# Kernel tuning notes

Hardware: AMD Instinct MI355X
Metric: run time of the kernel (lower is better)

The kernel has to match this reference:

```python
import jax, jax.numpy as jnp
import numpy as np

B, C, H, W = 16, 256, 64, 64
NH, HD, NM = 4, 32, 4  # heads, head_dim, memory tokens
HID = NH * HD


def rms_norm(x, g):
    # F.normalize(x, dim=1) * sqrt(C) * g  (channel dim = 1)
    norm = jnp.maximum(jnp.linalg.norm(x, axis=1, keepdims=True), 1e-12)
    return x / norm * (x.shape[1] ** 0.5) * g


def setup_inputs() -> dict:
    key = jax.random.key(0)
    ks = jax.random.split(key, 5)
    return {
        "x": jax.random.normal(ks[0], (B, C, H, W), jnp.float32),
        "g_in": jnp.ones((1, C, 1, 1), jnp.float32),
        "mem_kv": jax.random.normal(ks[1], (2, NH, HD, NM), jnp.float32),
        "w_qkv": jax.random.normal(ks[2], (HID * 3, C), jnp.float32) * (C ** -0.5),
        "w_out": jax.random.normal(ks[3], (C, HID), jnp.float32) * (HID ** -0.5),
        "b_out": jnp.zeros((C,), jnp.float32),
        "g_out": jnp.ones((1, C, 1, 1), jnp.float32),
    }


def reference(x, g_in, mem_kv, w_qkv, w_out, b_out, g_out):
    b, c, h, w = x.shape
    n = h * w
    scale = HD ** -0.5

    xn = rms_norm(x, g_in)
    # 1x1 conv as matmul over channel dim: [B, 3*HID, H, W]
    qkv = jnp.einsum('oc,bchw->bohw', w_qkv, xn)
    q, k, v = jnp.split(qkv, 3, axis=1)
    # b (h d) x y -> b h d n
    q = q.reshape(b, NH, HD, n)
    k = k.reshape(b, NH, HD, n)
    v = v.reshape(b, NH, HD, n)

    # prepend memory key/value tokens: [b, h, d, NM + n]
    mk = jnp.broadcast_to(mem_kv[0], (b, NH, HD, NM))
    mv = jnp.broadcast_to(mem_kv[1], (b, NH, HD, NM))
    k = jnp.concatenate([mk, k], axis=-1)
    v = jnp.concatenate([mv, v], axis=-1)

    q = jax.nn.softmax(q, axis=-2) * scale  # softmax over head_dim
    k = jax.nn.softmax(k, axis=-1)          # softmax over tokens

    context = jnp.einsum('bhdn,bhen->bhde', k, v)  # [b, h, d, e]
    out = jnp.einsum('bhde,bhdn->bhen', context, q)  # [b, h, e, n]
    out = out.reshape(b, HID, h, w)

    out = jnp.einsum('oc,bchw->bohw', w_out, out) + b_out[None, :, None, None]
    return rms_norm(out, g_out)
```

## Files before the change

kernel.cpp:

```cpp
#include <hip/hip_runtime.h>
#include <math.h>

typedef unsigned short u16;
typedef unsigned int u32;

#define NBATCH 16
#define NCH    256
#define NPIX   4096
#define NHEAD  4
#define HDIM   32
#define NMEM   4
#define HID    128
#define OC3    384
#define SCALE_Q 0.17677669529663687f

typedef __bf16 bf16x8 __attribute__((ext_vector_type(8)));
typedef float  f32x4  __attribute__((ext_vector_type(4)));

__device__ __forceinline__ u16 bfb(float f){
  union { __bf16 h; u16 u; } x; x.h = (__bf16)f; return x.u;
}
__device__ __forceinline__ u32 pkbf2(float a, float b){
  union { __bf16 h[2]; u32 u; } x; x.h[0] = (__bf16)a; x.h[1] = (__bf16)b; return x.u;
}
__device__ __forceinline__ void gload_lds16(const void* gp, void* lp){
  __builtin_amdgcn_global_load_lds(
      (const __attribute__((address_space(1))) unsigned int*)gp,
      (__attribute__((address_space(3))) unsigned int*)lp, 16, 0, 0);
}

__global__ __launch_bounds__(256) void k_pack(const float* __restrict__ wqkv,
                                              const float* __restrict__ gin,
                                              const float* __restrict__ wout,
                                              const float* __restrict__ memkv,
                                              u16* __restrict__ wqb,
                                              u16* __restrict__ wob,
                                              float* __restrict__ ctxmem,
                                              float* __restrict__ zmem)
{
  int i = blockIdx.x*256 + threadIdx.x;
  if (i < OC3*NCH){ int c = i & 255; wqb[i] = bfb(wqkv[i]*gin[c]); }
  else if (i < OC3*NCH + NCH*HID){ int j = i - OC3*NCH; wob[j] = bfb(wout[j]); }
  else {
    int j = i - (OC3*NCH + NCH*HID);
    if (j < 4096){
      int h = j>>10, d = (j>>5)&31, e = j&31;
      float s = 0.f;
      #pragma unroll
      for (int m=0;m<4;m++)
        s += __expf(memkv[(h*HDIM+d)*NMEM + m]) * memkv[512 + (h*HDIM+e)*NMEM + m];
      ctxmem[j] = s;
    } else if (j < 4224){
      int k = j - 4096; int h = k>>5, d = k&31;
      float s = 0.f;
      #pragma unroll
      for (int m=0;m<4;m++) s += __expf(memkv[(h*HDIM+d)*NMEM + m]);
      zmem[k] = s;
    }
  }
}

__global__ __launch_bounds__(512, 4) void k_qkvx(const float* __restrict__ x,
                                                 const u16* __restrict__ wqb,
                                                 u16* __restrict__ qt,
                                                 float* __restrict__ ctxp2)
{
  __shared__ __align__(16) char smem[52480];
  float (*Xs)[64]   = (float(*)[64])smem;
  u16*   Bx         = (u16*)(smem + 16384);
  float (*ssqp)[64] = (float(*)[64])(smem + 50176);
  float* rl         = (float*)(smem + 52224);
  u16*   Ek         = (u16*)smem;
  u16*   Vv         = (u16*)(smem + 18432);
  float (*psx)[64]  = (float(*)[64])(smem + 36864);

  const int t = threadIdx.x, w = t>>6, lane = t&63;
  const int n0 = blockIdx.x*64, b = blockIdx.y;
  const int qw = lane>>4, rr = lane&15;

  {
    float ssq = 0.f;
    for (int s=0;s<4;++s){
      asm volatile("s_waitcnt lgkmcnt(0)" ::: "memory");
      const float* gp = x + ((size_t)b*NCH + s*64 + w*8 + (lane>>4))*NPIX + n0 + (lane&15)*4;
      gload_lds16(gp,                    &Xs[w*8 + 0][0]);
      gload_lds16(gp + (size_t)4*NPIX,   &Xs[w*8 + 4][0]);
      asm volatile("s_waitcnt vmcnt(0)" ::: "memory");
      u32 pk[4];
      #pragma unroll
      for (int q=0;q<4;q++){
        float v0 = Xs[w*8 + 2*q    ][lane];
        float v1 = Xs[w*8 + 2*q + 1][lane];
        ssq += v0*v0 + v1*v1;
        pk[q] = pkbf2(v0, v1);
      }
      *(int4*)&Bx[lane*264 + s*64 + w*8] = make_int4((int)pk[0],(int)pk[1],(int)pk[2],(int)pk[3]);
    }
    ssqp[w][lane] = ssq;
  }
  __syncthreads();
  if (t < 64){
    float s = 0.f;
    #pragma unroll
    for (int g=0;g<8;g++) s += ssqp[g][t];
    rl[t] = 16.0f / fmaxf(sqrtf(s), 1e-12f);
  }

  f32x4 acc[3][4];
  #pragma unroll
  for (int p=0;p<3;p++)
    #pragma unroll
    for (int nf=0;nf<4;nf++) acc[p][nf] = (f32x4){0.f,0.f,0.f,0.f};

  const u16* aw = wqb + (size_t)(w*16 + rr)*NCH + qw*8;
  bf16x8 caf0 = *(const bf16x8*)(aw);
  bf16x8 caf1 = *(const bf16x8*)(aw + 128*NCH);
  bf16x8 caf2 = *(const bf16x8*)(aw + 256*NCH);
  #pragma unroll
  for (int c0=0; c0<NCH; c0+=32){
    bf16x8 bfr[4];
    #pragma unroll
    for (int nf=0;nf<4;nf++)
      bfr[nf] = *(const bf16x8*)&Bx[(nf*16+rr)*264 + c0 + qw*8];
    bf16x8 naf0 = caf0, naf1 = caf1, naf2 = caf2;
    if (c0 < NCH-32){
      naf0 = *(const bf16x8*)(aw + c0+32);
      naf1 = *(const bf16x8*)(aw + 128*NCH + c0+32);
      naf2 = *(const bf16x8*)(aw + 256*NCH + c0+32);
    }
    #pragma unroll
    for (int nf=0;nf<4;nf++){
      acc[0][nf] = __builtin_amdgcn_mfma_f32_16x16x32_bf16(caf0, bfr[nf], acc[0][nf], 0, 0, 0);
      acc[1][nf] = __builtin_amdgcn_mfma_f32_16x16x32_bf16(bfr[nf], caf1, acc[1][nf], 0, 0, 0);
      acc[2][nf] = __builtin_amdgcn_mfma_f32_16x16x32_bf16(bfr[nf], caf2, acc[2][nf], 0, 0, 0);
    }
    caf0 = naf0; caf1 = naf1; caf2 = naf2;
  }

  __syncthreads();

  float zk = 0.f;
  #pragma unroll
  for (int nf=0;nf<4;nf++){
    const float4 rv4 = *(const float4*)&rl[nf*16 + qw*4];
    float e0 = __expf(acc[1][nf][0]*rv4.x);
    float e1 = __expf(acc[1][nf][1]*rv4.y);
    float e2 = __expf(acc[1][nf][2]*rv4.z);
    float e3 = __expf(acc[1][nf][3]*rv4.w);
    zk += e0+e1+e2+e3;
    *(int2*)&Ek[(w*16+rr)*72 + nf*16 + qw*4] =
        make_int2((int)pkbf2(e0,e1), (int)pkbf2(e2,e3));
    float v0 = acc[2][nf][0]*rv4.x, v1 = acc[2][nf][1]*rv4.y;
    float v2 = acc[2][nf][2]*rv4.z, v3 = acc[2][nf][3]*rv4.w;
    *(int2*)&Vv[(w*16+rr)*72 + nf*16 + qw*4] =
        make_int2((int)pkbf2(v0,v1), (int)pkbf2(v2,v3));
  }
  zk += __shfl_xor(zk, 16, 64);
  zk += __shfl_xor(zk, 32, 64);

  float qv[4][4], pm[4], ps[4];
  #pragma unroll
  for (int nf=0;nf<4;nf++){
    float rv = rl[nf*16 + rr];
    float m = -1e30f;
    #pragma unroll
    for (int r=0;r<4;r++){ qv[nf][r] = acc[0][nf][r]*rv; m = fmaxf(m, qv[nf][r]); }
    m = fmaxf(m, __shfl_xor(m, 16, 64));
    m = fmaxf(m, __shfl_xor(m, 32, 64));
    float s = 0.f;
    #pragma unroll
    for (int r=0;r<4;r++){ qv[nf][r] = __expf(qv[nf][r]-m); s += qv[nf][r]; }
    s += __shfl_xor(s, 16, 64);
    s += __shfl_xor(s, 32, 64);
    pm[nf] = m; ps[nf] = s;
  }
  if (lane < 16){
    #pragma unroll
    for (int nf=0;nf<4;nf++){ ssqp[w][nf*16+lane] = pm[nf]; psx[w][nf*16+lane] = ps[nf]; }
  }
  __syncthreads();
  {
    const int pw = w^1;
    u16* qbase = qt + ((size_t)b*NPIX + n0)*HID + w*16 + qw*4;
    #pragma unroll
    for (int nf=0;nf<4;nf++){
      float om = ssqp[pw][nf*16+rr], os = psx[pw][nf*16+rr];
      float M = fmaxf(pm[nf], om);
      float S = ps[nf]*__expf(pm[nf]-M) + os*__expf(om-M);
      float f = __expf(pm[nf]-M) * SCALE_Q / S;
      u32 lo = pkbf2(qv[nf][0]*f, qv[nf][1]*f);
      u32 hi = pkbf2(qv[nf][2]*f, qv[nf][3]*f);
      *(int2*)(qbase + (size_t)(nf*16+rr)*HID) = make_int2((int)lo,(int)hi);
    }
  }

  {
    const int h = w>>1, eh = w&1;
    f32x4 pacc[2] = {(f32x4){0.f,0.f,0.f,0.f},(f32x4){0.f,0.f,0.f,0.f}};
    #pragma unroll
    for (int ks=0; ks<2; ks++){
      bf16x8 bv = *(const bf16x8*)&Vv[(h*32+eh*16+rr)*72 + ks*32 + qw*8];
      #pragma unroll
      for (int i=0;i<2;i++){
        bf16x8 ae = *(const bf16x8*)&Ek[(h*32+i*16+rr)*72 + ks*32 + qw*8];
        pacc[i] = __builtin_amdgcn_mfma_f32_16x16x32_bf16(ae, bv, pacc[i], 0, 0, 0);
      }
    }
    float* pb = ctxp2 + ((size_t)((b*64 + blockIdx.x)*4 + h))*1088;
    #pragma unroll
    for (int i=0;i<2;i++)
      #pragma unroll
      for (int reg=0;reg<4;reg++)
        pb[(i*16+qw*4+reg)*32 + eh*16 + rr] = pacc[i][reg];
    if (qw==0) pb[1024 + (w&1)*16 + rr] = zk;
  }
}

__global__ __launch_bounds__(256) void k_w2(const float* __restrict__ ctxp2,
                                            const float* __restrict__ ctxmem,
                                            const float* __restrict__ zmem,
                                            const u16* __restrict__ wob,
                                            u16* __restrict__ w2b)
{
  __shared__ u16 Ct[32][40];
  __shared__ float zps[8][32];
  __shared__ float rinv[32];
  const int bh = blockIdx.x, b = bh>>2, h = bh&3;
  const int t = threadIdx.x, w = t>>6, lane = t&63;
  const int qw = lane>>4, rr = lane&15;
  const int d = t>>3, e0 = (t&7)*4;

  const float* base = ctxp2 + ((size_t)(b*64)*4 + h)*1088;
  float4 ps = make_float4(0.f,0.f,0.f,0.f);
  for (int s=0;s<64;s++){
    float4 v = *(const float4*)(base + (size_t)s*4*1088 + d*32 + e0);
    ps.x+=v.x; ps.y+=v.y; ps.z+=v.z; ps.w+=v.w;
  }
  {
    int dz = t&31, sg = t>>5;
    float zp = 0.f;
    for (int s=sg*8; s<sg*8+8; s++) zp += base[(size_t)s*4*1088 + 1024 + dz];
    zps[sg][dz] = zp;
  }
  __syncthreads();
  if (t < 32){
    float z = zmem[h*32 + t];
    #pragma unroll
    for (int g=0;g<8;g++) z += zps[g][t];
    rinv[t] = 1.0f / z;
  }
  __syncthreads();
  {
    float ri = rinv[d];
    const float* cm = ctxmem + h*1024 + d*32 + e0;
    Ct[d][e0+0] = bfb((ps.x + cm[0])*ri);
    Ct[d][e0+1] = bfb((ps.y + cm[1])*ri);
    Ct[d][e0+2] = bfb((ps.z + cm[2])*ri);
    Ct[d][e0+3] = bfb((ps.w + cm[3])*ri);
  }
  __syncthreads();
  f32x4 pacc[4][2];
  #pragma unroll
  for (int mf=0;mf<4;mf++)
    #pragma unroll
    for (int nd=0;nd<2;nd++) pacc[mf][nd] = (f32x4){0.f,0.f,0.f,0.f};
  bf16x8 be[2];
  be[0] = *(const bf16x8*)&Ct[rr][qw*8];
  be[1] = *(const bf16x8*)&Ct[16+rr][qw*8];
  #pragma unroll
  for (int mf=0;mf<4;mf++){
    bf16x8 af = *(const bf16x8*)&wob[(size_t)(w*64+mf*16+rr)*HID + h*32 + qw*8];
    #pragma unroll
    for (int nd=0;nd<2;nd++)
      pacc[mf][nd] = __builtin_amdgcn_mfma_f32_16x16x32_bf16(af, be[nd], pacc[mf][nd], 0, 0, 0);
  }
  #pragma unroll
  for (int mf=0;mf<4;mf++)
    #pragma unroll
    for (int nd=0;nd<2;nd++)
      #pragma unroll
      for (int reg=0;reg<4;reg++)
        w2b[((size_t)b*NCH + w*64+mf*16+qw*4+reg)*HID + h*32 + nd*16 + rr] =
            bfb(pacc[mf][nd][reg]);
}

__global__ __launch_bounds__(256) void k_fout(const u16* __restrict__ qt,
                                              const u16* __restrict__ w2b,
                                              const float* __restrict__ bout,
                                              const float* __restrict__ gout,
                                              float* __restrict__ out)
{
  __shared__ float ssql[4][64];
  const int t = threadIdx.x, w = t>>6, lane = t&63;
  const int n0 = blockIdx.x*64, b = blockIdx.y;
  const int qw = lane>>4, rr = lane&15;

  f32x4 acc[4][4];
  #pragma unroll
  for (int i=0;i<4;i++)
    #pragma unroll
    for (int j=0;j<4;j++) acc[i][j] = (f32x4){0.f,0.f,0.f,0.f};

  const u16* qbase = qt + ((size_t)b*NPIX + n0)*HID;
  const u16* wbase = w2b + (size_t)b*NCH*HID;
  #pragma unroll
  for (int k0=0;k0<HID;k0+=32){
    bf16x8 bq[4], aw[4];
    #pragma unroll
    for (int nf=0;nf<4;nf++)
      bq[nf] = *(const bf16x8*)(qbase + (size_t)(nf*16+rr)*HID + k0 + qw*8);
    #pragma unroll
    for (int mf=0;mf<4;mf++)
      aw[mf] = *(const bf16x8*)(wbase + (size_t)(w*64+mf*16+rr)*HID + k0 + qw*8);
    #pragma unroll
    for (int mf=0;mf<4;mf++)
      #pragma unroll
      for (int nf=0;nf<4;nf++)
        acc[mf][nf] = __builtin_amdgcn_mfma_f32_16x16x32_bf16(bq[nf], aw[mf], acc[mf][nf], 0, 0, 0);
  }
  float psq[4][4] = {{0.f}};
  #pragma unroll
  for (int mf=0;mf<4;mf++){
    float bb = bout[w*64+mf*16+rr];
    #pragma unroll
    for (int nf=0;nf<4;nf++)
      #pragma unroll
      for (int reg=0;reg<4;reg++){
        float v = acc[mf][nf][reg] + bb;
        acc[mf][nf][reg] = v;
        psq[nf][reg] += v*v;
      }
  }
  #pragma unroll
  for (int nf=0;nf<4;nf++)
    #pragma unroll
    for (int reg=0;reg<4;reg++){
      psq[nf][reg] += __shfl_xor(psq[nf][reg], 1, 64);
      psq[nf][reg] += __shfl_xor(psq[nf][reg], 2, 64);
      psq[nf][reg] += __shfl_xor(psq[nf][reg], 4, 64);
      psq[nf][reg] += __shfl_xor(psq[nf][reg], 8, 64);
    }
  if (rr==0){
    #pragma unroll
    for (int nf=0;nf<4;nf++)
      #pragma unroll
      for (int reg=0;reg<4;reg++)
        ssql[w][nf*16+qw*4+reg] = psq[nf][reg];
  }
  __syncthreads();
  float4 rv4[4];
  #pragma unroll
  for (int nf=0;nf<4;nf++){
    float4 s0 = *(const float4*)&ssql[0][nf*16+qw*4];
    float4 s1 = *(const float4*)&ssql[1][nf*16+qw*4];
    float4 s2 = *(const float4*)&ssql[2][nf*16+qw*4];
    float4 s3 = *(const float4*)&ssql[3][nf*16+qw*4];
    rv4[nf].x = 16.0f / fmaxf(sqrtf(s0.x+s1.x+s2.x+s3.x), 1e-12f);
    rv4[nf].y = 16.0f / fmaxf(sqrtf(s0.y+s1.y+s2.y+s3.y), 1e-12f);
    rv4[nf].z = 16.0f / fmaxf(sqrtf(s0.z+s1.z+s2.z+s3.z), 1e-12f);
    rv4[nf].w = 16.0f / fmaxf(sqrtf(s0.w+s1.w+s2.w+s3.w), 1e-12f);
  }
  #pragma unroll
  for (int mf=0;mf<4;mf++){
    float g = gout[w*64+mf*16+rr];
    float* po = out + ((size_t)(b*NCH + w*64+mf*16+rr))*NPIX + n0;
    #pragma unroll
    for (int nf=0;nf<4;nf++){
      float4 o4;
      o4.x = acc[mf][nf][0]*rv4[nf].x*g;
      o4.y = acc[mf][nf][1]*rv4[nf].y*g;
      o4.z = acc[mf][nf][2]*rv4[nf].z*g;
      o4.w = acc[mf][nf][3]*rv4[nf].w*g;
      *(float4*)(po + nf*16 + qw*4) = o4;
    }
  }
}

extern "C" void kernel_launch(void* const* d_in, const int* in_sizes, int n_in,
                              void* d_out, int out_size, void* d_ws, size_t ws_size,
                              hipStream_t stream)
{
  const float* x     = (const float*)d_in[0];
  const float* gin   = (const float*)d_in[1];
  const float* memkv = (const float*)d_in[2];
  const float* wqkv  = (const float*)d_in[3];
  const float* wout  = (const float*)d_in[4];
  const float* bout  = (const float*)d_in[5];
  const float* gout  = (const float*)d_in[6];
  float* out = (float*)d_out;

  char* ws = (char*)d_ws;
  u16*    qt     = (u16*)   (ws);
  float*  ctxp2  = (float*) (ws + 16777216);
  u16*    w2b    = (u16*)   (ws + 34603008);
  float*  ctxmem = (float*) (ws + 35651584);
  float*  zmem   = (float*) (ws + 35667968);
  u16*    wqb    = (u16*)   (ws + 35668480);
  u16*    wob    = (u16*)   (ws + 35865088);

  hipLaunchKernelGGL(k_pack, dim3(529),   dim3(256), 0, stream,
                     wqkv, gin, wout, memkv, wqb, wob, ctxmem, zmem);
  hipLaunchKernelGGL(k_qkvx, dim3(64,16), dim3(512), 0, stream, x, wqb, qt, ctxp2);
  hipLaunchKernelGGL(k_w2,   dim3(64),    dim3(256), 0, stream,
                     ctxp2, ctxmem, zmem, wob, w2b);
  hipLaunchKernelGGL(k_fout, dim3(64,16), dim3(256), 0, stream,
                     qt, w2b, bout, gout, out);
}
```

Baseline: 178.8 us.

## Fuse context reduction into qkv kernel via last-block atomic, apply context in output kernel

Removes the separate k_w2 launch. The last block per batch, found with an atomic counter reset in k_pack, now reduces the partial contexts into a normalized bf16 context in k_qkvx. k_fout now applies context to q per head with MFMA, stages the result in LDS, then multiplies by w_out, instead of using a precomputed per-batch fused weight. This saves one kernel launch and the serialized small-grid k_w2. In exchange k_fout does extra MFMA and LDS work, and the tail block in k_qkvx carries a serial reduction.

```diff
diff --git a/kernel.cpp b/kernel.cpp
--- a/kernel.cpp
+++ b/kernel.cpp
@@ -36,7 +36,8 @@
                                               u16* __restrict__ wqb,
                                               u16* __restrict__ wob,
                                               float* __restrict__ ctxmem,
-                                              float* __restrict__ zmem)
+                                              float* __restrict__ zmem,
+                                              u32* __restrict__ cnt)
 {
   int i = blockIdx.x*256 + threadIdx.x;
   if (i < OC3*NCH){ int c = i & 255; wqb[i] = bfb(wqkv[i]*gin[c]); }
@@ -56,6 +57,8 @@
       #pragma unroll
       for (int m=0;m<4;m++) s += __expf(memkv[(h*HDIM+d)*NMEM + m]);
       zmem[k] = s;
+    } else if (j < 4240){
+      cnt[j-4224] = 0;
     }
   }
 }
@@ -63,7 +66,11 @@
 __global__ __launch_bounds__(512, 4) void k_qkvx(const float* __restrict__ x,
                                                  const u16* __restrict__ wqb,
                                                  u16* __restrict__ qt,
-                                                 float* __restrict__ ctxp2)
+                                                 float* __restrict__ ctxp2,
+                                                 const float* __restrict__ ctxmem,
+                                                 const float* __restrict__ zmem,
+                                                 u16* __restrict__ ctxn,
+                                                 u32* __restrict__ cnt)
 {
   __shared__ __align__(16) char smem[52480];
   float (*Xs)[64]   = (float(*)[64])smem;
@@ -73,6 +80,7 @@
   u16*   Ek         = (u16*)smem;
   u16*   Vv         = (u16*)(smem + 18432);
   float (*psx)[64]  = (float(*)[64])(smem + 36864);
+  __shared__ int lflag;
 
   const int t = threadIdx.x, w = t>>6, lane = t&63;
   const int n0 = blockIdx.x*64, b = blockIdx.y;
@@ -214,109 +222,109 @@
         pb[(i*16+qw*4+reg)*32 + eh*16 + rr] = pacc[i][reg];
     if (qw==0) pb[1024 + (w&1)*16 + rr] = zk;
   }
-}
-
-__global__ __launch_bounds__(256) void k_w2(const float* __restrict__ ctxp2,
-                                            const float* __restrict__ ctxmem,
-                                            const float* __restrict__ zmem,
-                                            const u16* __restrict__ wob,
-                                            u16* __restrict__ w2b)
-{
-  __shared__ u16 Ct[32][40];
-  __shared__ float zps[8][32];
-  __shared__ float rinv[32];
-  const int bh = blockIdx.x, b = bh>>2, h = bh&3;
-  const int t = threadIdx.x, w = t>>6, lane = t&63;
-  const int qw = lane>>4, rr = lane&15;
-  const int d = t>>3, e0 = (t&7)*4;
-
-  const float* base = ctxp2 + ((size_t)(b*64)*4 + h)*1088;
-  float4 ps = make_float4(0.f,0.f,0.f,0.f);
-  for (int s=0;s<64;s++){
-    float4 v = *(const float4*)(base + (size_t)s*4*1088 + d*32 + e0);
-    ps.x+=v.x; ps.y+=v.y; ps.z+=v.z; ps.w+=v.w;
-  }
+
+  __threadfence();
+  __syncthreads();
+  if (t == 0){
+    u32 old = __hip_atomic_fetch_add(cnt + b, 1u, __ATOMIC_ACQ_REL,
+                                     __HIP_MEMORY_SCOPE_AGENT);
+    lflag = (old == 63);
+  }
+  __syncthreads();
+  if (!lflag) return;
+  __threadfence();
+
+  float* rl2 = (float*)ssqp;
+  float (*zps)[128] = (float(*)[128])psx;
+  const float* cb = ctxp2 + (size_t)(b*64)*4*1088;
   {
-    int dz = t&31, sg = t>>5;
-    float zp = 0.f;
-    for (int s=sg*8; s<sg*8+8; s++) zp += base[(size_t)s*4*1088 + 1024 + dz];
-    zps[sg][dz] = zp;
-  }
-  __syncthreads();
-  if (t < 32){
-    float z = zmem[h*32 + t];
-    #pragma unroll
-    for (int g=0;g<8;g++) z += zps[g][t];
-    rinv[t] = 1.0f / z;
-  }
-  __syncthreads();
-  {
-    float ri = rinv[d];
-    const float* cm = ctxmem + h*1024 + d*32 + e0;
-    Ct[d][e0+0] = bfb((ps.x + cm[0])*ri);
-    Ct[d][e0+1] = bfb((ps.y + cm[1])*ri);
-    Ct[d][e0+2] = bfb((ps.z + cm[2])*ri);
-    Ct[d][e0+3] = bfb((ps.w + cm[3])*ri);
-  }
-  __syncthreads();
-  f32x4 pacc[4][2];
-  #pragma unroll
-  for (int mf=0;mf<4;mf++)
-    #pragma unroll
-    for (int nd=0;nd<2;nd++) pacc[mf][nd] = (f32x4){0.f,0.f,0.f,0.f};
-  bf16x8 be[2];
-  be[0] = *(const bf16x8*)&Ct[rr][qw*8];
-  be[1] = *(const bf16x8*)&Ct[16+rr][qw*8];
-  #pragma unroll
-  for (int mf=0;mf<4;mf++){
-    bf16x8 af = *(const bf16x8*)&wob[(size_t)(w*64+mf*16+rr)*HID + h*32 + qw*8];
-    #pragma unroll
-    for (int nd=0;nd<2;nd++)
-      pacc[mf][nd] = __builtin_amdgcn_mfma_f32_16x16x32_bf16(af, be[nd], pacc[mf][nd], 0, 0, 0);
-  }
-  #pragma unroll
-  for (int mf=0;mf<4;mf++)
-    #pragma unroll
-    for (int nd=0;nd<2;nd++)
-      #pragma unroll
-      for (int reg=0;reg<4;reg++)
-        w2b[((size_t)b*NCH + w*64+mf*16+qw*4+reg)*HID + h*32 + nd*16 + rr] =
-            bfb(pacc[mf][nd][reg]);
+    int sg = t>>7, idx = t&127;
+    int h = idx>>5, dd = idx&31;
+    const float* pz = cb + (size_t)h*1088 + 1024 + dd;
+    float zs = 0.f;
+    #pragma unroll
+    for (int s=0;s<16;s++) zs += pz[(size_t)(sg*16+s)*4*1088];
+    zps[sg][idx] = zs;
+  }
+  __syncthreads();
+  if (t < 128) rl2[t] = 1.0f/(zps[0][t]+zps[1][t]+zps[2][t]+zps[3][t]+zmem[t]);
+  __syncthreads();
+  #pragma unroll
+  for (int uu=0; uu<2; ++uu){
+    int u = t + uu*512;
+    int h = u>>8, dd = (u>>3)&31, e0 = (u&7)*4;
+    const float* pp = cb + (size_t)h*1088 + dd*32 + e0;
+    const float* cm = ctxmem + h*1024 + dd*32 + e0;
+    float4 s4 = make_float4(cm[0],cm[1],cm[2],cm[3]);
+    #pragma unroll
+    for (int s=0;s<64;s++){
+      float4 v = *(const float4*)(pp + (size_t)s*4*1088);
+      s4.x+=v.x; s4.y+=v.y; s4.z+=v.z; s4.w+=v.w;
+    }
+    float ri = rl2[h*32+dd];
+    u16* cn = ctxn + (size_t)b*4096 + h*1024 + dd;
+    cn[(e0+0)*32] = bfb(s4.x*ri);
+    cn[(e0+1)*32] = bfb(s4.y*ri);
+    cn[(e0+2)*32] = bfb(s4.z*ri);
+    cn[(e0+3)*32] = bfb(s4.w*ri);
+  }
 }
 
 __global__ __launch_bounds__(256) void k_fout(const u16* __restrict__ qt,
-                                              const u16* __restrict__ w2b,
+                                              const u16* __restrict__ ctxn,
+                                              const u16* __restrict__ wob,
                                               const float* __restrict__ bout,
                                               const float* __restrict__ gout,
                                               float* __restrict__ out)
 {
+  __shared__ u16 Ao[64*136];
   __shared__ float ssql[4][64];
   const int t = threadIdx.x, w = t>>6, lane = t&63;
   const int n0 = blockIdx.x*64, b = blockIdx.y;
   const int qw = lane>>4, rr = lane&15;
 
+  f32x4 pv[4][2];
+  const u16* qp  = qt + ((size_t)b*NPIX + n0 + w*16 + rr)*HID;
+  const u16* cnb = ctxn + (size_t)b*4096;
+  #pragma unroll
+  for (int h=0;h<4;h++){
+    bf16x8 bq = *(const bf16x8*)(qp + h*32 + qw*8);
+    #pragma unroll
+    for (int ef=0;ef<2;ef++){
+      bf16x8 af = *(const bf16x8*)(cnb + (size_t)(h*32 + ef*16 + rr)*32 + qw*8);
+      f32x4 z = (f32x4){0.f,0.f,0.f,0.f};
+      pv[h][ef] = __builtin_amdgcn_mfma_f32_16x16x32_bf16(af, bq, z, 0, 0, 0);
+    }
+  }
+  #pragma unroll
+  for (int h=0;h<4;h++)
+    #pragma unroll
+    for (int ef=0;ef<2;ef++){
+      u32 lohi0 = pkbf2(pv[h][ef][0], pv[h][ef][1]);
+      u32 lohi1 = pkbf2(pv[h][ef][2], pv[h][ef][3]);
+      *(int2*)&Ao[(w*16+rr)*136 + h*32 + ef*16 + qw*4] = make_int2((int)lohi0,(int)lohi1);
+    }
+  __syncthreads();
+
   f32x4 acc[4][4];
   #pragma unroll
   for (int i=0;i<4;i++)
     #pragma unroll
     for (int j=0;j<4;j++) acc[i][j] = (f32x4){0.f,0.f,0.f,0.f};
-
-  const u16* qbase = qt + ((size_t)b*NPIX + n0)*HID;
-  const u16* wbase = w2b + (size_t)b*NCH*HID;
-  #pragma unroll
-  for (int k0=0;k0<HID;k0+=32){
-    bf16x8 bq[4], aw[4];
+  #pragma unroll
+  for (int k0=0; k0<HID; k0+=32){
+    bf16x8 af[4], bfr[4];
+    #pragma unroll
+    for (int mf=0;mf<4;mf++)
+      af[mf] = *(const bf16x8*)&wob[(size_t)(w*64 + mf*16 + rr)*HID + k0 + qw*8];
     #pragma unroll
     for (int nf=0;nf<4;nf++)
-      bq[nf] = *(const bf16x8*)(qbase + (size_t)(nf*16+rr)*HID + k0 + qw*8);
+      bfr[nf] = *(const bf16x8*)&Ao[(nf*16+rr)*136 + k0 + qw*8];
     #pragma unroll
     for (int mf=0;mf<4;mf++)
-      aw[mf] = *(const bf16x8*)(wbase + (size_t)(w*64+mf*16+rr)*HID + k0 + qw*8);
-    #pragma unroll
-    for (int mf=0;mf<4;mf++)
       #pragma unroll
       for (int nf=0;nf<4;nf++)
-        acc[mf][nf] = __builtin_amdgcn_mfma_f32_16x16x32_bf16(bq[nf], aw[mf], acc[mf][nf], 0, 0, 0);
+        acc[mf][nf] = __builtin_amdgcn_mfma_f32_16x16x32_bf16(bfr[nf], af[mf], acc[mf][nf], 0, 0, 0);
   }
   float psq[4][4] = {{0.f}};
   #pragma unroll
@@ -392,17 +400,17 @@
   char* ws = (char*)d_ws;
   u16*    qt     = (u16*)   (ws);
   float*  ctxp2  = (float*) (ws + 16777216);
-  u16*    w2b    = (u16*)   (ws + 34603008);
-  float*  ctxmem = (float*) (ws + 35651584);
-  float*  zmem   = (float*) (ws + 35667968);
-  u16*    wqb    = (u16*)   (ws + 35668480);
-  u16*    wob    = (u16*)   (ws + 35865088);
+  u16*    ctxn   = (u16*)   (ws + 34603008);
+  float*  ctxmem = (float*) (ws + 34734080);
+  float*  zmem   = (float*) (ws + 34750464);
+  u32*    cnt    = (u32*)   (ws + 34750976);
+  u16*    wqb    = (u16*)   (ws + 34751232);
+  u16*    wob    = (u16*)   (ws + 34947840);
 
   hipLaunchKernelGGL(k_pack, dim3(529),   dim3(256), 0, stream,
-                     wqkv, gin, wout, memkv, wqb, wob, ctxmem, zmem);
-  hipLaunchKernelGGL(k_qkvx, dim3(64,16), dim3(512), 0, stream, x, wqb, qt, ctxp2);
-  hipLaunchKernelGGL(k_w2,   dim3(64),    dim3(256), 0, stream,
-                     ctxp2, ctxmem, zmem, wob, w2b);
+                     wqkv, gin, wout, memkv, wqb, wob, ctxmem, zmem, cnt);
+  hipLaunchKernelGGL(k_qkvx, dim3(64,16), dim3(512), 0, stream,
+                     x, wqb, qt, ctxp2, ctxmem, zmem, ctxn, cnt);
   hipLaunchKernelGGL(k_fout, dim3(64,16), dim3(256), 0, stream,
-                     qt, w2b, bout, gout, out);
-}
+                     qt, ctxn, wob, bout, gout, out);
+}
```

After: 528.8 us. 2.96x slower.
